# Kernel tuning notes

Hardware: AMD Instinct MI355X
Metric: run time of the kernel (lower is better)

Reference implementation:

```python
import jax, jax.numpy as jnp
import numpy as np

N_NODES = 100000
N_EDGES = 1000000
D_IN = 64
EDGE_DIM = 16
D_OUT = 64


def setup_inputs() -> dict:
    key = jax.random.key(0)
    ks = jax.random.split(key, 8)
    x = jax.random.normal(ks[0], (N_NODES, D_IN), dtype=jnp.float32)
    edge_attr = jax.random.normal(ks[1], (N_EDGES, EDGE_DIM), dtype=jnp.float32)
    W_e = jax.random.normal(ks[2], (EDGE_DIM, D_IN), dtype=jnp.float32) / np.sqrt(EDGE_DIM)
    b_e = jax.random.normal(ks[3], (D_IN,), dtype=jnp.float32) * 0.01
    W_l = jax.random.normal(ks[4], (D_IN, D_OUT), dtype=jnp.float32) / np.sqrt(D_IN)
    b_l = jax.random.normal(ks[5], (D_OUT,), dtype=jnp.float32) * 0.01
    W_r = jax.random.normal(ks[6], (D_IN, D_OUT), dtype=jnp.float32) / np.sqrt(D_IN)
    edge_index = jax.random.randint(ks[7], (2, N_EDGES), 0, N_NODES, dtype=jnp.int64)
    return {"x": x, "edge_attr": edge_attr, "W_e": W_e, "b_e": b_e,
            "W_l": W_l, "b_l": b_l, "W_r": W_r, "edge_index": edge_index}


def reference(x, edge_attr, W_e, b_e, W_l, b_l, W_r, edge_index):
    # EdgeSAGEConv with edge_agg='add', aggr='mean', root_weight=True
    n = x.shape[0]
    src, dst = edge_index[0], edge_index[1]  # PyG: row0 = source j, row1 = target i
    # message: x_j + map_edges(edge_attr)
    msg = x[src] + (edge_attr @ W_e + b_e)            # [E, D_IN]
    # scatter-mean aggregate at target nodes
    agg = jax.ops.segment_sum(msg, dst, num_segments=n)             # [N, D_IN]
    cnt = jax.ops.segment_sum(jnp.ones((msg.shape[0], 1), msg.dtype), dst,
                              num_segments=n)                        # [N, 1]
    agg = agg / jnp.maximum(cnt, 1.0)
    # lin_l(agg) + lin_r(x)
    return agg @ W_l + b_l + x @ W_r
```

## Files before the change

kernel.cpp:

```cpp
#include <hip/hip_runtime.h>

#define D 64
#define ED 16

__global__ void detect_idx64_kernel(const int* __restrict__ idx32, int* __restrict__ flag)
{
    __shared__ int any;
    if (threadIdx.x == 0) any = 0;
    __syncthreads();
    int v = 0;
    for (int i = threadIdx.x; i < 8192; i += blockDim.x)
        v |= idx32[2 * i + 1];
    if (v) atomicOr(&any, 1);
    __syncthreads();
    if (threadIdx.x == 0) flag[0] = (any == 0) ? 1 : 0;
}

__device__ __forceinline__ int load_idx(const void* p, size_t i, int is64)
{
    return is64 ? (int)((const long long*)p)[i] : ((const int*)p)[i];
}

__global__ void __launch_bounds__(256)
count_kernel(const void* __restrict__ edge_index, const int* __restrict__ flag,
             int* __restrict__ cnt, int n_edges)
{
    const int is64 = flag[0];
    const int stride = gridDim.x * blockDim.x;
    for (int e = blockIdx.x * blockDim.x + threadIdx.x; e < n_edges; e += stride) {
        int dst = load_idx(edge_index, (size_t)n_edges + e, is64);
        atomicAdd(&cnt[dst], 1);
    }
}

__global__ void scan1_kernel(const int* __restrict__ cnt, int* __restrict__ offs,
                             int* __restrict__ bsum, int n)
{
    __shared__ int sd[256];
    const int t = threadIdx.x;
    const int i = blockIdx.x * 256 + t;
    int v = (i < n) ? cnt[i] : 0;
    sd[t] = v;
    __syncthreads();
    for (int off = 1; off < 256; off <<= 1) {
        int add = (t >= off) ? sd[t - off] : 0;
        __syncthreads();
        sd[t] += add;
        __syncthreads();
    }
    if (i < n) offs[i] = sd[t] - v;
    if (t == 255) bsum[blockIdx.x] = sd[t];
}

__global__ void scan2_kernel(int* __restrict__ bsum, int nb)
{
    __shared__ int sd[512];
    const int t = threadIdx.x;
    int v = (t < nb) ? bsum[t] : 0;
    sd[t] = v;
    __syncthreads();
    for (int off = 1; off < 512; off <<= 1) {
        int add = (t >= off) ? sd[t - off] : 0;
        __syncthreads();
        sd[t] += add;
        __syncthreads();
    }
    if (t < nb) bsum[t] = sd[t] - v;
}

__global__ void scan3_kernel(int* __restrict__ offs, int* __restrict__ cursor,
                             const int* __restrict__ bsum, int n, int n_edges)
{
    const int i = blockIdx.x * 256 + threadIdx.x;
    if (i < n) {
        int v = offs[i] + bsum[i >> 8];
        offs[i]   = v;
        cursor[i] = v;
    }
    if (i == 0) offs[n] = n_edges;
}

__global__ void __launch_bounds__(256)
scatter_kernel(const void* __restrict__ edge_index, const int* __restrict__ flag,
               int* __restrict__ cursor, int2* __restrict__ pair, int n_edges)
{
    const int is64 = flag[0];
    const int stride = gridDim.x * blockDim.x;
    for (int e = blockIdx.x * blockDim.x + threadIdx.x; e < n_edges; e += stride) {
        int src = load_idx(edge_index, e, is64);
        int dst = load_idx(edge_index, (size_t)n_edges + e, is64);
        int pos = atomicAdd(&cursor[dst], 1);
        pair[pos] = make_int2(src, e);
    }
}

__global__ void __launch_bounds__(256)
reduce_kernel(const float* __restrict__ x,
              const float* __restrict__ edge_attr,
              const float* __restrict__ W_e,
              const float* __restrict__ b_e,
              const int2* __restrict__ pair,
              const int* __restrict__ offs,
              float* __restrict__ agg,
              int n_nodes)
{
    const int lane = threadIdx.x & 63;
    const int wid  = threadIdx.x >> 6;
    const int sub  = lane >> 4;
    const int k16  = lane & 15;

    float Wreg[ED];
    #pragma unroll
    for (int k = 0; k < ED; ++k) Wreg[k] = W_e[k * D + lane];
    const float beL = b_e[lane];

    const int nstride = gridDim.x * 4;
    for (int node = blockIdx.x * 4 + wid; node < n_nodes; node += nstride) {
        const int beg = offs[node];
        const int deg = offs[node + 1] - beg;

        float xs  = 0.0f;
        float eas = 0.0f;

        for (int j0 = 0; j0 < deg; j0 += 16) {
            const int nb = min(16, deg - j0);
            int2 p = make_int2(0, 0);
            if (lane < nb) p = pair[beg + j0 + lane];

            float t[16];
            #pragma unroll
            for (int m = 0; m < 16; ++m) {
                int s = __shfl(p.x, m);
                t[m] = (m < nb) ? x[(size_t)s * D + lane] : 0.0f;
            }

            #pragma unroll
            for (int mm = 0; mm < 4; ++mm) {
                int m = sub + 4 * mm;
                int eid = __shfl(p.y, m);
                if (m < nb) eas += edge_attr[(size_t)eid * ED + k16];
            }

            #pragma unroll
            for (int m = 0; m < 16; ++m) xs += t[m];
        }

        float ea2 = eas + __shfl_xor(eas, 16);
        ea2 += __shfl_xor(ea2, 32);

        float acc = xs + (float)deg * beL;
        #pragma unroll
        for (int k = 0; k < ED; ++k)
            acc += __shfl(ea2, k) * Wreg[k];

        agg[(size_t)node * D + lane] = acc * (1.0f / fmaxf((float)deg, 1.0f));
    }
}

__global__ void __launch_bounds__(256)
edge_scatter_kernel(const float* __restrict__ x,
                    const float* __restrict__ edge_attr,
                    const float* __restrict__ W_e,
                    const float* __restrict__ b_e,
                    const void* __restrict__ edge_index,
                    const int* __restrict__ flag,
                    float* __restrict__ agg,
                    float* __restrict__ cnt,
                    int n_edges)
{
    __shared__ float We[ED * D];
    __shared__ float be[D];
    for (int i = threadIdx.x; i < ED * D; i += blockDim.x) We[i] = W_e[i];
    if (threadIdx.x < D) be[threadIdx.x] = b_e[threadIdx.x];
    __syncthreads();

    const int is64 = flag[0];
    const int lane = threadIdx.x & 63;
    const int wid  = threadIdx.x >> 6;
    const int estr = gridDim.x * 4;

    for (int e = blockIdx.x * 4 + wid; e < n_edges; e += estr) {
        int src = load_idx(edge_index, e, is64);
        int dst = load_idx(edge_index, (size_t)n_edges + e, is64);
        const float4* ea = (const float4*)(edge_attr + (size_t)e * ED);
        float4 e0 = ea[0], e1 = ea[1], e2 = ea[2], e3 = ea[3];

        float m = be[lane] + x[(size_t)src * D + lane];
        m += e0.x * We[ 0*D + lane] + e0.y * We[ 1*D + lane]
           + e0.z * We[ 2*D + lane] + e0.w * We[ 3*D + lane];
        m += e1.x * We[ 4*D + lane] + e1.y * We[ 5*D + lane]
           + e1.z * We[ 6*D + lane] + e1.w * We[ 7*D + lane];
        m += e2.x * We[ 8*D + lane] + e2.y * We[ 9*D + lane]
           + e2.z * We[10*D + lane] + e2.w * We[11*D + lane];
        m += e3.x * We[12*D + lane] + e3.y * We[13*D + lane]
           + e3.z * We[14*D + lane] + e3.w * We[15*D + lane];

        atomicAdd(&agg[(size_t)dst * D + lane], m);
        if (lane == 0) atomicAdd(&cnt[dst], 1.0f);
    }
}

__global__ void divide_kernel(float* __restrict__ agg, const float* __restrict__ cnt, int n_nodes)
{
    const int i = blockIdx.x * 256 + threadIdx.x;
    if (i < n_nodes * D) {
        float c = cnt[i >> 6];
        agg[i] *= 1.0f / fmaxf(c, 1.0f);
    }
}

#define BM 128
#define BK 32
#define ATP 132

__global__ void __launch_bounds__(256, 4)
node_gemm_kernel(const float* x,
                 const float* agg,
                 const float* __restrict__ W_l,
                 const float* __restrict__ b_l,
                 const float* __restrict__ W_r,
                 float* out,
                 int n_nodes)
{
    __shared__ float AT[BK][ATP];
    __shared__ float Wt[BK][D];

    const int t   = threadIdx.x;
    const int to  = t & 15;
    const int tm  = t >> 4;
    const int base = blockIdx.x * BM;

    float acc[8][4];
    #pragma unroll
    for (int n = 0; n < 8; ++n)
        #pragma unroll
        for (int c = 0; c < 4; ++c) acc[n][c] = 0.0f;

    #pragma unroll 1
    for (int s = 0; s < 4; ++s) {
        const float* src  = (s < 2) ? agg : x;
        const float* Wsrc = (s < 2) ? W_l : W_r;
        const int    k0   = (s & 1) * BK;

        __syncthreads();

        #pragma unroll
        for (int q = 0; q < 4; ++q) {
            const int idx  = t + 256 * q;
            const int node = idx >> 3;
            const int kq   = (idx & 7) * 4;
            float4 v = make_float4(0.f, 0.f, 0.f, 0.f);
            if (base + node < n_nodes)
                v = *(const float4*)(src + (size_t)(base + node) * D + k0 + kq);
            AT[kq + 0][node] = v.x;
            AT[kq + 1][node] = v.y;
            AT[kq + 2][node] = v.z;
            AT[kq + 3][node] = v.w;
        }
        #pragma unroll
        for (int q = 0; q < 2; ++q) {
            const int idx = t + 256 * q;
            const int kk  = idx >> 4;
            const int cq  = (idx & 15) * 4;
            *(float4*)&Wt[kk][cq] = *(const float4*)(Wsrc + (size_t)(k0 + kk) * D + cq);
        }
        __syncthreads();

        #pragma unroll 4
        for (int kk = 0; kk < BK; ++kk) {
            float4 a0 = *(const float4*)&AT[kk][tm * 8];
            float4 a1 = *(const float4*)&AT[kk][tm * 8 + 4];
            float4 w  = *(const float4*)&Wt[kk][to * 4];
            acc[0][0] += a0.x * w.x; acc[0][1] += a0.x * w.y; acc[0][2] += a0.x * w.z; acc[0][3] += a0.x * w.w;
            acc[1][0] += a0.y * w.x; acc[1][1] += a0.y * w.y; acc[1][2] += a0.y * w.z; acc[1][3] += a0.y * w.w;
            acc[2][0] += a0.z * w.x; acc[2][1] += a0.z * w.y; acc[2][2] += a0.z * w.z; acc[2][3] += a0.z * w.w;
            acc[3][0] += a0.w * w.x; acc[3][1] += a0.w * w.y; acc[3][2] += a0.w * w.z; acc[3][3] += a0.w * w.w;
            acc[4][0] += a1.x * w.x; acc[4][1] += a1.x * w.y; acc[4][2] += a1.x * w.z; acc[4][3] += a1.x * w.w;
            acc[5][0] += a1.y * w.x; acc[5][1] += a1.y * w.y; acc[5][2] += a1.y * w.z; acc[5][3] += a1.y * w.w;
            acc[6][0] += a1.z * w.x; acc[6][1] += a1.z * w.y; acc[6][2] += a1.z * w.z; acc[6][3] += a1.z * w.w;
            acc[7][0] += a1.w * w.x; acc[7][1] += a1.w * w.y; acc[7][2] += a1.w * w.z; acc[7][3] += a1.w * w.w;
        }
    }

    const float4 bb = *(const float4*)(b_l + to * 4);
    #pragma unroll
    for (int n = 0; n < 8; ++n) {
        const int node = base + tm * 8 + n;
        if (node < n_nodes) {
            float4 r = make_float4(acc[n][0] + bb.x, acc[n][1] + bb.y,
                                   acc[n][2] + bb.z, acc[n][3] + bb.w);
            *(float4*)(out + (size_t)node * D + to * 4) = r;
        }
    }
}

extern "C" void kernel_launch(void* const* d_in, const int* in_sizes, int n_in,
                              void* d_out, int out_size, void* d_ws, size_t ws_size,
                              hipStream_t stream)
{
    const float* x         = (const float*)d_in[0];
    const float* edge_attr = (const float*)d_in[1];
    const float* W_e       = (const float*)d_in[2];
    const float* b_e       = (const float*)d_in[3];
    const float* W_l       = (const float*)d_in[4];
    const float* b_l       = (const float*)d_in[5];
    const float* W_r       = (const float*)d_in[6];
    const void*  edge_index= d_in[7];

    const int n_nodes = in_sizes[0] / D;
    const int n_edges = in_sizes[1] / ED;

    float* out = (float*)d_out;

    const size_t n_align = ((size_t)n_nodes + 255) & ~(size_t)255;
    const int    NB      = (n_nodes + 255) / 256;
    const size_t o_flag  = 0;
    const size_t o_cnt   = 512;
    const size_t o_offs  = o_cnt  + n_align * 4;
    const size_t o_cur   = o_offs + n_align * 4 + 256;
    const size_t o_bsum  = o_cur  + n_align * 4;
    const size_t o_pair  = (o_bsum + (size_t)NB * 4 + 255) & ~(size_t)255;
    const size_t need    = o_pair + (size_t)n_edges * 8;

    int* flag = (int*)((char*)d_ws + o_flag);

    detect_idx64_kernel<<<1, 256, 0, stream>>>((const int*)edge_index, flag);

    if (need <= ws_size && NB <= 512) {
        int*  cnt    = (int*)((char*)d_ws + o_cnt);
        int*  offs   = (int*)((char*)d_ws + o_offs);
        int*  cursor = (int*)((char*)d_ws + o_cur);
        int*  bsum   = (int*)((char*)d_ws + o_bsum);
        int2* pair   = (int2*)((char*)d_ws + o_pair);

        hipMemsetAsync(cnt, 0, n_align * 4, stream);

        count_kernel<<<2048, 256, 0, stream>>>(edge_index, flag, cnt, n_edges);
        scan1_kernel<<<NB, 256, 0, stream>>>(cnt, offs, bsum, n_nodes);
        scan2_kernel<<<1, 512, 0, stream>>>(bsum, NB);
        scan3_kernel<<<NB, 256, 0, stream>>>(offs, cursor, bsum, n_nodes, n_edges);
        scatter_kernel<<<2048, 256, 0, stream>>>(edge_index, flag, cursor, pair, n_edges);
        reduce_kernel<<<2048, 256, 0, stream>>>(
            x, edge_attr, W_e, b_e, pair, offs, out, n_nodes);
    } else {
        float* cntf = (float*)((char*)d_ws + o_cnt);
        hipMemsetAsync(out, 0, (size_t)out_size * sizeof(float), stream);
        hipMemsetAsync(cntf, 0, (size_t)n_nodes * sizeof(float), stream);
        edge_scatter_kernel<<<4096, 256, 0, stream>>>(
            x, edge_attr, W_e, b_e, edge_index, flag, out, cntf, n_edges);
        divide_kernel<<<(n_nodes * D + 255) / 256, 256, 0, stream>>>(out, cntf, n_nodes);
    }

    node_gemm_kernel<<<(n_nodes + BM - 1) / BM, 256, 0, stream>>>(
        x, out, W_l, b_l, W_r, out, n_nodes);
}
```

Measured before the change: 252.8 us.

## Gather neighbor features from a bf16 copy of x in the CSR reduce

Adds a pre-pass that converts x to bf16 with round-to-nearest-even into workspace. A new reduce kernel gathers the bf16 rows, so each neighbor read is 128 bytes instead of 256, and processes two neighbors per wave-instruction. It also sums the raw edge attributes first and applies W_e once per node (linearity) rather than per edge. This halves the random-gather traffic at the cost of an extra conversion pass and reduced precision in the aggregated features.

```diff
diff --git a/kernel.cpp b/kernel.cpp
--- a/kernel.cpp
+++ b/kernel.cpp
@@ -2,6 +2,9 @@
 
 #define D 64
 #define ED 16
+
+typedef unsigned short ushort_t;
+typedef unsigned int uint_t;
 
 __global__ void detect_idx64_kernel(const int* __restrict__ idx32, int* __restrict__ flag)
 {
@@ -21,6 +24,28 @@
     return is64 ? (int)((const long long*)p)[i] : ((const int*)p)[i];
 }
 
+__device__ __forceinline__ ushort_t f2bf_rne(float f)
+{
+    uint_t u = __float_as_uint(f);
+    u = (u + 0x7FFFu + ((u >> 16) & 1u)) >> 16;
+    return (ushort_t)u;
+}
+
+__global__ void __launch_bounds__(256)
+xconv_kernel(const float* __restrict__ x, uint_t* __restrict__ xb, int n4)
+{
+    const int stride = gridDim.x * blockDim.x;
+    for (int i = blockIdx.x * blockDim.x + threadIdx.x; i < n4; i += stride) {
+        float4 a = ((const float4*)x)[2 * i];
+        float4 b = ((const float4*)x)[2 * i + 1];
+        uint_t r0 = ((uint_t)f2bf_rne(a.y) << 16) | f2bf_rne(a.x);
+        uint_t r1 = ((uint_t)f2bf_rne(a.w) << 16) | f2bf_rne(a.z);
+        uint_t r2 = ((uint_t)f2bf_rne(b.y) << 16) | f2bf_rne(b.x);
+        uint_t r3 = ((uint_t)f2bf_rne(b.w) << 16) | f2bf_rne(b.z);
+        ((uint4*)xb)[i] = make_uint4(r0, r1, r2, r3);
+    }
+}
+
 __global__ void __launch_bounds__(256)
 count_kernel(const void* __restrict__ edge_index, const int* __restrict__ flag,
              int* __restrict__ cnt, int n_edges)
@@ -91,6 +116,89 @@
         int dst = load_idx(edge_index, (size_t)n_edges + e, is64);
         int pos = atomicAdd(&cursor[dst], 1);
         pair[pos] = make_int2(src, e);
+    }
+}
+
+__global__ void __launch_bounds__(256)
+reduce_bf16_kernel(const uint_t* __restrict__ xb,
+                   const float* __restrict__ edge_attr,
+                   const float* __restrict__ W_e,
+                   const float* __restrict__ b_e,
+                   const int2* __restrict__ pair,
+                   const int* __restrict__ offs,
+                   float* __restrict__ agg,
+                   int n_nodes)
+{
+    const int lane = threadIdx.x & 63;
+    const int wid  = threadIdx.x >> 6;
+    const int half = lane >> 5;
+    const int c    = lane & 31;
+    const int sub  = lane >> 4;
+    const int k16  = lane & 15;
+
+    float W0[ED], W1[ED];
+    #pragma unroll
+    for (int k = 0; k < ED; ++k) {
+        W0[k] = W_e[k * D + 2 * c];
+        W1[k] = W_e[k * D + 2 * c + 1];
+    }
+    const float be0 = b_e[2 * c];
+    const float be1 = b_e[2 * c + 1];
+
+    const int nstride = gridDim.x * 4;
+    for (int node = blockIdx.x * 4 + wid; node < n_nodes; node += nstride) {
+        const int beg = offs[node];
+        const int deg = offs[node + 1] - beg;
+
+        float xs0 = 0.0f, xs1 = 0.0f;
+        float eas = 0.0f;
+
+        for (int j0 = 0; j0 < deg; j0 += 16) {
+            const int nb = min(16, deg - j0);
+            int2 p = make_int2(0, 0);
+            if (lane < nb) p = pair[beg + j0 + lane];
+
+            uint_t u[8];
+            #pragma unroll
+            for (int r = 0; r < 8; ++r) {
+                int s = __shfl(p.x, 2 * r + half);
+                u[r] = 0;
+                if (2 * r < nb)
+                    u[r] = xb[(size_t)s * 32 + c];
+            }
+
+            #pragma unroll
+            for (int mm = 0; mm < 4; ++mm) {
+                int m = sub + 4 * mm;
+                int eid = __shfl(p.y, m);
+                if (m < nb) eas += edge_attr[(size_t)eid * ED + k16];
+            }
+
+            #pragma unroll
+            for (int r = 0; r < 8; ++r) {
+                if (2 * r + half < nb) {
+                    xs0 += __uint_as_float(u[r] << 16);
+                    xs1 += __uint_as_float(u[r] & 0xFFFF0000u);
+                }
+            }
+        }
+
+        float ea2 = eas + __shfl_xor(eas, 16);
+        ea2 += __shfl_xor(ea2, 32);
+        xs0 += __shfl_xor(xs0, 32);
+        xs1 += __shfl_xor(xs1, 32);
+
+        float a0 = xs0 + (float)deg * be0;
+        float a1 = xs1 + (float)deg * be1;
+        #pragma unroll
+        for (int k = 0; k < ED; ++k) {
+            float e = __shfl(ea2, k);
+            a0 += e * W0[k];
+            a1 += e * W1[k];
+        }
+        const float sc = 1.0f / fmaxf((float)deg, 1.0f);
+        if (half == 0)
+            *(float2*)(agg + (size_t)node * D + 2 * c) = make_float2(a0 * sc, a1 * sc);
     }
 }
 
@@ -321,6 +429,8 @@
     const size_t o_bsum  = o_cur  + n_align * 4;
     const size_t o_pair  = (o_bsum + (size_t)NB * 4 + 255) & ~(size_t)255;
     const size_t need    = o_pair + (size_t)n_edges * 8;
+    const size_t o_xb    = (need + 255) & ~(size_t)255;
+    const size_t need_bf = o_xb + (size_t)n_nodes * D * 2;
 
     int* flag = (int*)((char*)d_ws + o_flag);
 
@@ -332,16 +442,26 @@
         int*  cursor = (int*)((char*)d_ws + o_cur);
         int*  bsum   = (int*)((char*)d_ws + o_bsum);
         int2* pair   = (int2*)((char*)d_ws + o_pair);
+        uint_t* xb   = (uint_t*)((char*)d_ws + o_xb);
+        const bool use_bf = (need_bf <= ws_size) && ((n_nodes * D) % 8 == 0);
 
         hipMemsetAsync(cnt, 0, n_align * 4, stream);
+
+        if (use_bf)
+            xconv_kernel<<<2048, 256, 0, stream>>>(x, xb, n_nodes * D / 8);
 
         count_kernel<<<2048, 256, 0, stream>>>(edge_index, flag, cnt, n_edges);
         scan1_kernel<<<NB, 256, 0, stream>>>(cnt, offs, bsum, n_nodes);
         scan2_kernel<<<1, 512, 0, stream>>>(bsum, NB);
         scan3_kernel<<<NB, 256, 0, stream>>>(offs, cursor, bsum, n_nodes, n_edges);
         scatter_kernel<<<2048, 256, 0, stream>>>(edge_index, flag, cursor, pair, n_edges);
-        reduce_kernel<<<2048, 256, 0, stream>>>(
-            x, edge_attr, W_e, b_e, pair, offs, out, n_nodes);
+
+        if (use_bf)
+            reduce_bf16_kernel<<<2048, 256, 0, stream>>>(
+                xb, edge_attr, W_e, b_e, pair, offs, out, n_nodes);
+        else
+            reduce_kernel<<<2048, 256, 0, stream>>>(
+                x, edge_attr, W_e, b_e, pair, offs, out, n_nodes);
     } else {
         float* cntf = (float*)((char*)d_ws + o_cnt);
         hipMemsetAsync(out, 0, (size_t)out_size * sizeof(float), stream);
```

Result: slower. 258.1 us (+2.1%).

## Batch four nodes per wavefront in reduce kernel to raise memory-level parallelism

Applied to the files above, without the earlier changes.

Each wavefront in the reduce kernel now handles four destination nodes at once. It issues all first-chunk gathers of x rows and edge attributes for those nodes before reducing them, and any remaining chunks are processed per node afterward. The goal is to keep more independent global loads in flight and hide gather latency. The cost is much higher register pressure (64 gathered floats plus four pair loads), which may lower occupancy. The launch_bounds(256) annotation is removed, so the compiler is free to allocate more registers.

```diff
diff --git a/kernel.cpp b/kernel.cpp
--- a/kernel.cpp
+++ b/kernel.cpp
@@ -94,7 +94,54 @@
     }
 }
 
-__global__ void __launch_bounds__(256)
+#define GATHER_X(J)                                                         \
+    _Pragma("unroll")                                                       \
+    for (int m = 0; m < 16; ++m) {                                          \
+        int s = __shfl(p##J.x, m);                                          \
+        t##J[m] = (m < nb##J) ? x[(size_t)s * D + lane] : 0.0f;             \
+    }
+
+#define GATHER_EA(J)                                                        \
+    _Pragma("unroll")                                                       \
+    for (int mm = 0; mm < 4; ++mm) {                                        \
+        int m = sub + 4 * mm;                                               \
+        int eid = __shfl(p##J.y, m);                                        \
+        if (m < nb##J) eac##J += edge_attr[(size_t)eid * ED + k16];         \
+    }
+
+#define FINISH(J) do {                                                      \
+    float xs = 0.0f;                                                        \
+    _Pragma("unroll")                                                       \
+    for (int m = 0; m < 16; ++m) xs += t##J[m];                             \
+    for (int j0 = 16; j0 < deg##J; j0 += 16) {               \
+        const int nbt = min(16, deg##J - j0);                               \
+        int2 pt = make_int2(0, 0);                                          \
+        if (lane < nbt) pt = pair[beg##J + j0 + lane];                      \
+        float tt[16];                                                       \
+        _Pragma("unroll")                                                   \
+        for (int m = 0; m < 16; ++m) {                                      \
+            int s = __shfl(pt.x, m);                                        \
+            tt[m] = (m < nbt) ? x[(size_t)s * D + lane] : 0.0f;             \
+        }                                                                   \
+        _Pragma("unroll")                                                   \
+        for (int mm = 0; mm < 4; ++mm) {                                    \
+            int m = sub + 4 * mm;                                           \
+            int eid = __shfl(pt.y, m);                                      \
+            if (m < nbt) eac##J += edge_attr[(size_t)eid * ED + k16];       \
+        }                                                                   \
+        _Pragma("unroll")                                                   \
+        for (int m = 0; m < 16; ++m) xs += tt[m];                           \
+    }                                                                       \
+    float eaf = eac##J + __shfl_xor(eac##J, 16);                            \
+    eaf += __shfl_xor(eaf, 32);                                             \
+    float acc = xs + (float)deg##J * beL;                                   \
+    _Pragma("unroll")                                                       \
+    for (int k = 0; k < ED; ++k) acc += __shfl(eaf, k) * Wreg[k];           \
+    if (v##J)                                                               \
+        agg[(size_t)n##J * D + lane] = acc * (1.0f / fmaxf((float)deg##J, 1.0f)); \
+} while (0)
+
+__global__ void
 reduce_kernel(const float* __restrict__ x,
               const float* __restrict__ edge_attr,
               const float* __restrict__ W_e,
@@ -114,46 +161,46 @@
     for (int k = 0; k < ED; ++k) Wreg[k] = W_e[k * D + lane];
     const float beL = b_e[lane];
 
-    const int nstride = gridDim.x * 4;
-    for (int node = blockIdx.x * 4 + wid; node < n_nodes; node += nstride) {
-        const int beg = offs[node];
-        const int deg = offs[node + 1] - beg;
-
-        float xs  = 0.0f;
-        float eas = 0.0f;
-
-        for (int j0 = 0; j0 < deg; j0 += 16) {
-            const int nb = min(16, deg - j0);
-            int2 p = make_int2(0, 0);
-            if (lane < nb) p = pair[beg + j0 + lane];
-
-            float t[16];
-            #pragma unroll
-            for (int m = 0; m < 16; ++m) {
-                int s = __shfl(p.x, m);
-                t[m] = (m < nb) ? x[(size_t)s * D + lane] : 0.0f;
-            }
-
-            #pragma unroll
-            for (int mm = 0; mm < 4; ++mm) {
-                int m = sub + 4 * mm;
-                int eid = __shfl(p.y, m);
-                if (m < nb) eas += edge_attr[(size_t)eid * ED + k16];
-            }
-
-            #pragma unroll
-            for (int m = 0; m < 16; ++m) xs += t[m];
-        }
-
-        float ea2 = eas + __shfl_xor(eas, 16);
-        ea2 += __shfl_xor(ea2, 32);
-
-        float acc = xs + (float)deg * beL;
-        #pragma unroll
-        for (int k = 0; k < ED; ++k)
-            acc += __shfl(ea2, k) * Wreg[k];
-
-        agg[(size_t)node * D + lane] = acc * (1.0f / fmaxf((float)deg, 1.0f));
+    const int tw = gridDim.x * 4;
+    const int wg = blockIdx.x * 4 + wid;
+
+    for (int k0 = 0; wg + k0 * tw < n_nodes; k0 += 4) {
+        const int  n0 = wg + (k0 + 0) * tw;
+        const int  n1 = wg + (k0 + 1) * tw;
+        const int  n2 = wg + (k0 + 2) * tw;
+        const int  n3 = wg + (k0 + 3) * tw;
+        const bool v0 = true;
+        const bool v1 = n1 < n_nodes;
+        const bool v2 = n2 < n_nodes;
+        const bool v3 = n3 < n_nodes;
+        const int  c1 = v1 ? n1 : 0;
+        const int  c2 = v2 ? n2 : 0;
+        const int  c3 = v3 ? n3 : 0;
+
+        const int beg0 = offs[n0], end0 = offs[n0 + 1];
+        const int beg1 = offs[c1], end1 = offs[c1 + 1];
+        const int beg2 = offs[c2], end2 = offs[c2 + 1];
+        const int beg3 = offs[c3], end3 = offs[c3 + 1];
+        const int deg0 = end0 - beg0;
+        const int deg1 = v1 ? (end1 - beg1) : 0;
+        const int deg2 = v2 ? (end2 - beg2) : 0;
+        const int deg3 = v3 ? (end3 - beg3) : 0;
+        const int nb0 = min(deg0, 16);
+        const int nb1 = min(deg1, 16);
+        const int nb2 = min(deg2, 16);
+        const int nb3 = min(deg3, 16);
+
+        int2 p0 = make_int2(0, 0); if (lane < nb0) p0 = pair[beg0 + lane];
+        int2 p1 = make_int2(0, 0); if (lane < nb1) p1 = pair[beg1 + lane];
+        int2 p2 = make_int2(0, 0); if (lane < nb2) p2 = pair[beg2 + lane];
+        int2 p3 = make_int2(0, 0); if (lane < nb3) p3 = pair[beg3 + lane];
+
+        float t0[16], t1[16], t2[16], t3[16];
+        float eac0 = 0.0f, eac1 = 0.0f, eac2 = 0.0f, eac3 = 0.0f;
+        GATHER_X(0); GATHER_X(1); GATHER_X(2); GATHER_X(3);
+        GATHER_EA(0); GATHER_EA(1); GATHER_EA(2); GATHER_EA(3);
+
+        FINISH(0); FINISH(1); FINISH(2); FINISH(3);
     }
 }
 
```

Result: slower. 286.8 us (+13.5%).

## Fuse node GEMM into CSR reduce, inline index-width detection, merge scan stages

Applied to the files above, without the earlier changes.

Folds the lin_l/lin_r projections into the per-node reduce kernel, so each wave keeps W_l and W_r columns in registers and computes the output row with shuffles. This removes the separate node_gemm pass and the write-then-read of the aggregate. It also drops the one-block detect kernel by checking the index width per wave inside each kernel, and replaces the single-block scan2 with a per-block prefix reduction in scan3. The trade-offs are heavy register use (128 weight floats per lane, with launch_bounds(256,1)), which may limit occupancy for the gather-bound loop, and a 64x64 shuffle-FMA loop per node instead of a tiled GEMM.

```diff
diff --git a/kernel.cpp b/kernel.cpp
--- a/kernel.cpp
+++ b/kernel.cpp
@@ -3,17 +3,10 @@
 #define D 64
 #define ED 16
 
-__global__ void detect_idx64_kernel(const int* __restrict__ idx32, int* __restrict__ flag)
-{
-    __shared__ int any;
-    if (threadIdx.x == 0) any = 0;
-    __syncthreads();
-    int v = 0;
-    for (int i = threadIdx.x; i < 8192; i += blockDim.x)
-        v |= idx32[2 * i + 1];
-    if (v) atomicOr(&any, 1);
-    __syncthreads();
-    if (threadIdx.x == 0) flag[0] = (any == 0) ? 1 : 0;
+__device__ __forceinline__ int detect_is64(const int* __restrict__ idx32)
+{
+    int v = idx32[2 * (threadIdx.x & 63) + 1];
+    return __all(v == 0) ? 1 : 0;
 }
 
 __device__ __forceinline__ int load_idx(const void* p, size_t i, int is64)
@@ -22,10 +15,9 @@
 }
 
 __global__ void __launch_bounds__(256)
-count_kernel(const void* __restrict__ edge_index, const int* __restrict__ flag,
-             int* __restrict__ cnt, int n_edges)
-{
-    const int is64 = flag[0];
+count_kernel(const void* __restrict__ edge_index, int* __restrict__ cnt, int n_edges)
+{
+    const int is64 = detect_is64((const int*)edge_index);
     const int stride = gridDim.x * blockDim.x;
     for (int e = blockIdx.x * blockDim.x + threadIdx.x; e < n_edges; e += stride) {
         int dst = load_idx(edge_index, (size_t)n_edges + e, is64);
@@ -52,28 +44,22 @@
     if (t == 255) bsum[blockIdx.x] = sd[t];
 }
 
-__global__ void scan2_kernel(int* __restrict__ bsum, int nb)
-{
-    __shared__ int sd[512];
-    const int t = threadIdx.x;
-    int v = (t < nb) ? bsum[t] : 0;
-    sd[t] = v;
-    __syncthreads();
-    for (int off = 1; off < 512; off <<= 1) {
-        int add = (t >= off) ? sd[t - off] : 0;
-        __syncthreads();
-        sd[t] += add;
-        __syncthreads();
-    }
-    if (t < nb) bsum[t] = sd[t] - v;
-}
-
 __global__ void scan3_kernel(int* __restrict__ offs, int* __restrict__ cursor,
                              const int* __restrict__ bsum, int n, int n_edges)
 {
+    __shared__ int red[256];
+    int part = 0;
+    for (int j = threadIdx.x; j < blockIdx.x; j += 256) part += bsum[j];
+    red[threadIdx.x] = part;
+    __syncthreads();
+    for (int off = 128; off > 0; off >>= 1) {
+        if (threadIdx.x < off) red[threadIdx.x] += red[threadIdx.x + off];
+        __syncthreads();
+    }
+    const int S = red[0];
     const int i = blockIdx.x * 256 + threadIdx.x;
     if (i < n) {
-        int v = offs[i] + bsum[i >> 8];
+        int v = offs[i] + S;
         offs[i]   = v;
         cursor[i] = v;
     }
@@ -81,10 +67,10 @@
 }
 
 __global__ void __launch_bounds__(256)
-scatter_kernel(const void* __restrict__ edge_index, const int* __restrict__ flag,
+scatter_kernel(const void* __restrict__ edge_index,
                int* __restrict__ cursor, int2* __restrict__ pair, int n_edges)
 {
-    const int is64 = flag[0];
+    const int is64 = detect_is64((const int*)edge_index);
     const int stride = gridDim.x * blockDim.x;
     for (int e = blockIdx.x * blockDim.x + threadIdx.x; e < n_edges; e += stride) {
         int src = load_idx(edge_index, e, is64);
@@ -94,28 +80,41 @@
     }
 }
 
-__global__ void __launch_bounds__(256)
-reduce_kernel(const float* __restrict__ x,
-              const float* __restrict__ edge_attr,
-              const float* __restrict__ W_e,
-              const float* __restrict__ b_e,
-              const int2* __restrict__ pair,
-              const int* __restrict__ offs,
-              float* __restrict__ agg,
-              int n_nodes)
+__global__ void __launch_bounds__(256, 1)
+fused_kernel(const float* __restrict__ x,
+             const float* __restrict__ edge_attr,
+             const float* __restrict__ W_e,
+             const float* __restrict__ b_e,
+             const float* __restrict__ W_l,
+             const float* __restrict__ b_l,
+             const float* __restrict__ W_r,
+             const int2* __restrict__ pair,
+             const int* __restrict__ offs,
+             float* __restrict__ out,
+             int n_nodes)
 {
     const int lane = threadIdx.x & 63;
     const int wid  = threadIdx.x >> 6;
     const int sub  = lane >> 4;
     const int k16  = lane & 15;
 
-    float Wreg[ED];
+    float We[ED];
     #pragma unroll
-    for (int k = 0; k < ED; ++k) Wreg[k] = W_e[k * D + lane];
+    for (int k = 0; k < ED; ++k) We[k] = W_e[k * D + lane];
     const float beL = b_e[lane];
 
-    const int nstride = gridDim.x * 4;
-    for (int node = blockIdx.x * 4 + wid; node < n_nodes; node += nstride) {
+    float Wl[D], Wr[D];
+    #pragma unroll
+    for (int d = 0; d < D; ++d) {
+        Wl[d] = W_l[d * D + lane];
+        Wr[d] = W_r[d * D + lane];
+    }
+    const float blL = b_l[lane];
+
+    const int tw = gridDim.x * 4;
+    const int wg = blockIdx.x * 4 + wid;
+
+    for (int node = wg; node < n_nodes; node += tw) {
         const int beg = offs[node];
         const int deg = offs[node + 1] - beg;
 
@@ -151,9 +150,15 @@
         float acc = xs + (float)deg * beL;
         #pragma unroll
         for (int k = 0; k < ED; ++k)
-            acc += __shfl(ea2, k) * Wreg[k];
-
-        agg[(size_t)node * D + lane] = acc * (1.0f / fmaxf((float)deg, 1.0f));
+            acc += __shfl(ea2, k) * We[k];
+        acc *= 1.0f / fmaxf((float)deg, 1.0f);
+
+        const float xr = x[(size_t)node * D + lane];
+        float o = blL;
+        #pragma unroll
+        for (int d = 0; d < D; ++d)
+            o += __shfl(acc, d) * Wl[d] + __shfl(xr, d) * Wr[d];
+        out[(size_t)node * D + lane] = o;
     }
 }
 
@@ -163,7 +168,6 @@
                     const float* __restrict__ W_e,
                     const float* __restrict__ b_e,
                     const void* __restrict__ edge_index,
-                    const int* __restrict__ flag,
                     float* __restrict__ agg,
                     float* __restrict__ cnt,
                     int n_edges)
@@ -174,7 +178,7 @@
     if (threadIdx.x < D) be[threadIdx.x] = b_e[threadIdx.x];
     __syncthreads();
 
-    const int is64 = flag[0];
+    const int is64 = detect_is64((const int*)edge_index);
     const int lane = threadIdx.x & 63;
     const int wid  = threadIdx.x >> 6;
     const int estr = gridDim.x * 4;
@@ -314,19 +318,14 @@
 
     const size_t n_align = ((size_t)n_nodes + 255) & ~(size_t)255;
     const int    NB      = (n_nodes + 255) / 256;
-    const size_t o_flag  = 0;
-    const size_t o_cnt   = 512;
+    const size_t o_cnt   = 0;
     const size_t o_offs  = o_cnt  + n_align * 4;
     const size_t o_cur   = o_offs + n_align * 4 + 256;
     const size_t o_bsum  = o_cur  + n_align * 4;
     const size_t o_pair  = (o_bsum + (size_t)NB * 4 + 255) & ~(size_t)255;
     const size_t need    = o_pair + (size_t)n_edges * 8;
 
-    int* flag = (int*)((char*)d_ws + o_flag);
-
-    detect_idx64_kernel<<<1, 256, 0, stream>>>((const int*)edge_index, flag);
-
-    if (need <= ws_size && NB <= 512) {
+    if (need <= ws_size && NB <= 65536) {
         int*  cnt    = (int*)((char*)d_ws + o_cnt);
         int*  offs   = (int*)((char*)d_ws + o_offs);
         int*  cursor = (int*)((char*)d_ws + o_cur);
@@ -335,22 +334,20 @@
 
         hipMemsetAsync(cnt, 0, n_align * 4, stream);
 
-        count_kernel<<<2048, 256, 0, stream>>>(edge_index, flag, cnt, n_edges);
+        count_kernel<<<2048, 256, 0, stream>>>(edge_index, cnt, n_edges);
         scan1_kernel<<<NB, 256, 0, stream>>>(cnt, offs, bsum, n_nodes);
-        scan2_kernel<<<1, 512, 0, stream>>>(bsum, NB);
         scan3_kernel<<<NB, 256, 0, stream>>>(offs, cursor, bsum, n_nodes, n_edges);
-        scatter_kernel<<<2048, 256, 0, stream>>>(edge_index, flag, cursor, pair, n_edges);
-        reduce_kernel<<<2048, 256, 0, stream>>>(
-            x, edge_attr, W_e, b_e, pair, offs, out, n_nodes);
+        scatter_kernel<<<2048, 256, 0, stream>>>(edge_index, cursor, pair, n_edges);
+        fused_kernel<<<2048, 256, 0, stream>>>(
+            x, edge_attr, W_e, b_e, W_l, b_l, W_r, pair, offs, out, n_nodes);
     } else {
         float* cntf = (float*)((char*)d_ws + o_cnt);
         hipMemsetAsync(out, 0, (size_t)out_size * sizeof(float), stream);
         hipMemsetAsync(cntf, 0, (size_t)n_nodes * sizeof(float), stream);
         edge_scatter_kernel<<<4096, 256, 0, stream>>>(
-            x, edge_attr, W_e, b_e, edge_index, flag, out, cntf, n_edges);
+            x, edge_attr, W_e, b_e, edge_index, out, cntf, n_edges);
         divide_kernel<<<(n_nodes * D + 255) / 256, 256, 0, stream>>>(out, cntf, n_nodes);
-    }
-
-    node_gemm_kernel<<<(n_nodes + BM - 1) / BM, 256, 0, stream>>>(
-        x, out, W_l, b_l, W_r, out, n_nodes);
-}
+        node_gemm_kernel<<<(n_nodes + BM - 1) / BM, 256, 0, stream>>>(
+            x, out, W_l, b_l, W_r, out, n_nodes);
+    }
+}
```

Result: slower. 370.5 us (+46.6%).
